# Optimization experiments

Hardware: AMD Instinct MI355X
Metric: run time of the kernel (lower is better)

The kernel has to match this reference:

```python
import jax, jax.numpy as jnp
import numpy as np

DIM = 2048
S = 4           # num_residual_streams
V = 1           # num_input_views
LAYER_INDEX = 3
B = 4           # batch
N = 2048        # seq len
EPS = 1e-5


def setup_inputs() -> dict:
    key = jax.random.key(0)
    k0, = jax.random.split(key, 1)
    residuals = jax.random.normal(k0, (B * S, N, DIM), dtype=jnp.float32)
    # parameters, initialized as in the torch module
    norm_weight = jnp.ones((DIM,), dtype=jnp.float32)
    static_beta = jnp.ones((S,), dtype=jnp.float32)
    init_alpha0 = jnp.zeros((S, V), dtype=jnp.float32).at[LAYER_INDEX % S, :].set(1.0)
    static_alpha = jnp.concatenate([init_alpha0, jnp.eye(S, dtype=jnp.float32)], axis=1)  # (S, V+S)
    dynamic_alpha_fn = jnp.zeros((DIM, S + V), dtype=jnp.float32)
    dynamic_alpha_scale = jnp.float32(0.01)
    dynamic_beta_fn = jnp.zeros((DIM,), dtype=jnp.float32)
    dynamic_beta_scale = jnp.float32(0.01)
    return {
        "residuals": residuals,
        "norm_weight": norm_weight,
        "static_beta": static_beta,
        "static_alpha": static_alpha,
        "dynamic_alpha_fn": dynamic_alpha_fn,
        "dynamic_alpha_scale": dynamic_alpha_scale,
        "dynamic_beta_fn": dynamic_beta_fn,
        "dynamic_beta_scale": dynamic_beta_scale,
    }


def _layernorm(x, weight):
    mu = jnp.mean(x, axis=-1, keepdims=True)
    var = jnp.mean(jnp.square(x - mu), axis=-1, keepdims=True)
    return (x - mu) * jax.lax.rsqrt(var + EPS) * weight


def reference(residuals, norm_weight, static_beta, static_alpha,
              dynamic_alpha_fn, dynamic_alpha_scale,
              dynamic_beta_fn, dynamic_beta_scale):
    # ---- prepare ----
    # (b s) n d -> b n s d
    r = residuals.reshape(B, S, N, DIM).transpose(0, 2, 1, 3)  # (b, n, s, d)
    normed = _layernorm(r, norm_weight)
    wc_weight = jnp.tanh(normed @ dynamic_alpha_fn)            # (b, n, s, s+v)
    alpha = wc_weight * dynamic_alpha_scale + static_alpha     # (b, n, s, s+v)
    dc_weight = jnp.tanh(normed @ dynamic_beta_fn)             # (b, n, s)
    beta = dc_weight * dynamic_beta_scale + static_beta        # (b, n, s)
    mix_h = jnp.einsum('bnst,bnsd->bntd', alpha, r)            # (b, n, s+v, d)
    branch_input = mix_h[..., 0, :]                            # (b, n, d)  (views == 1)
    mixed_residuals = mix_h[..., 1:, :]                        # (b, n, s, d)
    # ---- forward (branch output fed back; identity branch) ----
    out = jnp.einsum('bnd,bns->bnsd', branch_input, beta) + mixed_residuals
    # b n s d -> (b s) n d
    return out.transpose(0, 2, 1, 3).reshape(B * S, N, DIM)
```

## Files before the change

kernel.cpp:

```cpp
#include <hip/hip_runtime.h>
#include <cstddef>

namespace {
constexpr int kDim = 2048;
constexpr int kS = 4;
constexpr int kSV = 5;
constexpr int kB = 4;
constexpr int kN = 2048;
constexpr float kEps = 1e-5f;
constexpr int kThreads = 256;
constexpr int kWaves = kThreads / 64;
}

__global__ __launch_bounds__(kThreads) void hyperconn_kernel(
    const float* __restrict__ res,
    const float* __restrict__ norm_w,
    const float* __restrict__ static_beta,
    const float* __restrict__ static_alpha,
    const float* __restrict__ alpha_fn,
    const float* __restrict__ alpha_scale_p,
    const float* __restrict__ beta_fn,
    const float* __restrict__ beta_scale_p,
    float* __restrict__ out)
{
  const int bid = blockIdx.x;
  const int b = bid / kN;
  const int n = bid % kN;
  const int tid = threadIdx.x;
  const int lane = tid & 63;
  const int wave = tid >> 6;

  __shared__ float red[kWaves][24];
  __shared__ float ab[24];

  const size_t plane = (size_t)kN * kDim;
  const float* base = res + (size_t)b * kS * plane + (size_t)n * kDim;
  float* obase      = out + (size_t)b * kS * plane + (size_t)n * kDim;

  const int d0 = tid * 4;
  const int d1 = tid * 4 + 1024;

  float r[kS][8];
  float wv[8];
#pragma unroll
  for (int s = 0; s < kS; ++s) {
    const float* rp = base + (size_t)s * plane;
    const float4 a = *(const float4*)(rp + d0);
    const float4 c = *(const float4*)(rp + d1);
    r[s][0] = a.x; r[s][1] = a.y; r[s][2] = a.z; r[s][3] = a.w;
    r[s][4] = c.x; r[s][5] = c.y; r[s][6] = c.z; r[s][7] = c.w;
  }
  {
    const float4 a = *(const float4*)(norm_w + d0);
    const float4 c = *(const float4*)(norm_w + d1);
    wv[0] = a.x; wv[1] = a.y; wv[2] = a.z; wv[3] = a.w;
    wv[4] = c.x; wv[5] = c.y; wv[6] = c.z; wv[7] = c.w;
  }

  float p1[8];
#pragma unroll
  for (int s = 0; s < kS; ++s) {
    float sm = 0.f, sq = 0.f;
#pragma unroll
    for (int j = 0; j < 8; ++j) { sm += r[s][j]; sq += r[s][j] * r[s][j]; }
    p1[2 * s] = sm;
    p1[2 * s + 1] = sq;
  }
#pragma unroll
  for (int k = 0; k < 8; ++k) {
#pragma unroll
    for (int off = 32; off > 0; off >>= 1)
      p1[k] += __shfl_xor(p1[k], off, 64);
  }
  if (lane == 0) {
#pragma unroll
    for (int k = 0; k < 8; ++k) red[wave][k] = p1[k];
  }
  __syncthreads();
#pragma unroll
  for (int k = 0; k < 8; ++k)
    p1[k] = red[0][k] + red[1][k] + red[2][k] + red[3][k];
  __syncthreads();

  float mu[kS], rstd[kS];
#pragma unroll
  for (int s = 0; s < kS; ++s) {
    const float m = p1[2 * s] * (1.f / kDim);
    const float var = p1[2 * s + 1] * (1.f / kDim) - m * m;
    mu[s] = m;
    rstd[s] = rsqrtf(var + kEps);
  }

  float p2[24];
#pragma unroll
  for (int k = 0; k < 24; ++k) p2[k] = 0.f;
#pragma unroll
  for (int half = 0; half < 2; ++half) {
#pragma unroll
    for (int j = 0; j < 4; ++j) {
      const int idx = half * 4 + j;
      const int d = (half ? d1 : d0) + j;
      const float a0 = alpha_fn[(size_t)d * kSV + 0];
      const float a1 = alpha_fn[(size_t)d * kSV + 1];
      const float a2 = alpha_fn[(size_t)d * kSV + 2];
      const float a3 = alpha_fn[(size_t)d * kSV + 3];
      const float a4 = alpha_fn[(size_t)d * kSV + 4];
      const float bv = beta_fn[d];
#pragma unroll
      for (int s = 0; s < kS; ++s) {
        const float nm = (r[s][idx] - mu[s]) * rstd[s] * wv[idx];
        p2[s * 6 + 0] = fmaf(nm, a0, p2[s * 6 + 0]);
        p2[s * 6 + 1] = fmaf(nm, a1, p2[s * 6 + 1]);
        p2[s * 6 + 2] = fmaf(nm, a2, p2[s * 6 + 2]);
        p2[s * 6 + 3] = fmaf(nm, a3, p2[s * 6 + 3]);
        p2[s * 6 + 4] = fmaf(nm, a4, p2[s * 6 + 4]);
        p2[s * 6 + 5] = fmaf(nm, bv, p2[s * 6 + 5]);
      }
    }
  }
#pragma unroll
  for (int k = 0; k < 24; ++k) {
#pragma unroll
    for (int off = 32; off > 0; off >>= 1)
      p2[k] += __shfl_xor(p2[k], off, 64);
  }
  if (lane == 0) {
#pragma unroll
    for (int k = 0; k < 24; ++k) red[wave][k] = p2[k];
  }
  __syncthreads();

  if (tid < 24) {
    const float tot = red[0][tid] + red[1][tid] + red[2][tid] + red[3][tid];
    const int s = tid / 6;
    const int q = tid % 6;
    const float t = tanhf(tot);
    float val;
    if (q < 5) val = fmaf(t, alpha_scale_p[0], static_alpha[s * kSV + q]);
    else       val = fmaf(t, beta_scale_p[0], static_beta[s]);
    ab[tid] = val;
  }
  __syncthreads();

  float al[kS][kSV], be[kS];
#pragma unroll
  for (int s = 0; s < kS; ++s) {
#pragma unroll
    for (int t = 0; t < kSV; ++t) al[s][t] = ab[s * 6 + t];
    be[s] = ab[s * 6 + 5];
  }

#pragma unroll
  for (int half = 0; half < 2; ++half) {
    const int dd = half ? d1 : d0;
    float4 ov[kS];
#pragma unroll
    for (int j = 0; j < 4; ++j) {
      const int idx = half * 4 + j;
      const float r0 = r[0][idx], r1 = r[1][idx], r2 = r[2][idx], r3 = r[3][idx];
      const float mix0 = al[0][0] * r0 + al[1][0] * r1 + al[2][0] * r2 + al[3][0] * r3;
#pragma unroll
      for (int so = 0; so < kS; ++so) {
        float t = al[0][so + 1] * r0 + al[1][so + 1] * r1 +
                  al[2][so + 1] * r2 + al[3][so + 1] * r3;
        t = fmaf(be[so], mix0, t);
        (&ov[so].x)[j] = t;
      }
    }
#pragma unroll
    for (int so = 0; so < kS; ++so)
      *(float4*)(obase + (size_t)so * plane + dd) = ov[so];
  }
}

extern "C" void kernel_launch(void* const* d_in, const int* in_sizes, int n_in,
                              void* d_out, int out_size, void* d_ws, size_t ws_size,
                              hipStream_t stream) {
  const float* res    = (const float*)d_in[0];
  const float* norm_w = (const float*)d_in[1];
  const float* sbeta  = (const float*)d_in[2];
  const float* salpha = (const float*)d_in[3];
  const float* afn    = (const float*)d_in[4];
  const float* ascale = (const float*)d_in[5];
  const float* bfn    = (const float*)d_in[6];
  const float* bscale = (const float*)d_in[7];
  float* outp = (float*)d_out;

  hipLaunchKernelGGL(hyperconn_kernel, dim3(kB * kN), dim3(kThreads), 0, stream,
                     res, norm_w, sbeta, salpha, afn, ascale, bfn, bscale, outp);
}
```

Measured before the change: 490.4 us.

## Fold norm weight into projection and merge layernorm stats with projection reduction

A tiny setup kernel precomputes norm_weight times alpha_fn and beta_fn in a transposed, vectorizable workspace layout, along with the column sums. The main kernel then accumulates sum, sum of squares and raw dot products in one pass. It recovers the normalized projections algebraically as (dot - mu*colsum)*rstd, which removes one block-wide reduction and barrier. It also replaces 32 separate butterfly reductions with a transposing shuffle reduction. The cost is an extra launch, a workspace dependency, and slightly different numerical rounding.

New measurement: 447.9 us. 1.09x faster.

```diff
diff --git a/kernel.cpp b/kernel.cpp
--- a/kernel.cpp
+++ b/kernel.cpp
@@ -10,17 +10,200 @@
 constexpr float kEps = 1e-5f;
 constexpr int kThreads = 256;
 constexpr int kWaves = kThreads / 64;
-}
-
-__global__ __launch_bounds__(kThreads) void hyperconn_kernel(
+constexpr int kNV = 32;
+constexpr size_t kWcElems = 6 * (size_t)kDim;
+constexpr size_t kWsNeeded = (kWcElems + 6) * sizeof(float);
+}
+
+__global__ __launch_bounds__(256) void hyperconn_setup(
+    const float* __restrict__ norm_w,
+    const float* __restrict__ alpha_fn,
+    const float* __restrict__ beta_fn,
+    float* __restrict__ ws)
+{
+  const int tid = threadIdx.x;
+  const int lane = tid & 63;
+  const int wave = tid >> 6;
+  __shared__ float red[4][6];
+
+  float acc[6] = {0.f, 0.f, 0.f, 0.f, 0.f, 0.f};
+#pragma unroll
+  for (int rep = 0; rep < kDim / 256; ++rep) {
+    const int d = rep * 256 + tid;
+    const float w = norm_w[d];
+    float c[6];
+    c[0] = alpha_fn[(size_t)d * kSV + 0];
+    c[1] = alpha_fn[(size_t)d * kSV + 1];
+    c[2] = alpha_fn[(size_t)d * kSV + 2];
+    c[3] = alpha_fn[(size_t)d * kSV + 3];
+    c[4] = alpha_fn[(size_t)d * kSV + 4];
+    c[5] = beta_fn[d];
+#pragma unroll
+    for (int t = 0; t < 6; ++t) {
+      const float wc = w * c[t];
+      ws[(size_t)t * kDim + d] = wc;
+      acc[t] += wc;
+    }
+  }
+#pragma unroll
+  for (int t = 0; t < 6; ++t) {
+#pragma unroll
+    for (int off = 32; off > 0; off >>= 1)
+      acc[t] += __shfl_xor(acc[t], off, 64);
+  }
+  if (lane == 0) {
+#pragma unroll
+    for (int t = 0; t < 6; ++t) red[wave][t] = acc[t];
+  }
+  __syncthreads();
+  if (tid < 6)
+    ws[kWcElems + tid] = red[0][tid] + red[1][tid] + red[2][tid] + red[3][tid];
+}
+
+__global__ __launch_bounds__(kThreads) void hyperconn_main(
     const float* __restrict__ res,
-    const float* __restrict__ norm_w,
     const float* __restrict__ static_beta,
     const float* __restrict__ static_alpha,
-    const float* __restrict__ alpha_fn,
     const float* __restrict__ alpha_scale_p,
-    const float* __restrict__ beta_fn,
     const float* __restrict__ beta_scale_p,
+    const float* __restrict__ ws,
+    float* __restrict__ out)
+{
+  const int bid = blockIdx.x;
+  const int b = bid >> 11;
+  const int n = bid & (kN - 1);
+  const int tid = threadIdx.x;
+  const int lane = tid & 63;
+  const int wave = tid >> 6;
+
+  __shared__ float red[kWaves][kNV];
+  __shared__ float ab[24];
+
+  const size_t plane = (size_t)kN * kDim;
+  const float* base = res + (size_t)b * kS * plane + (size_t)n * kDim;
+  float* obase      = out + (size_t)b * kS * plane + (size_t)n * kDim;
+
+  const int d0 = tid * 4;
+  const int d1 = tid * 4 + 1024;
+
+  float r[kS][8];
+#pragma unroll
+  for (int s = 0; s < kS; ++s) {
+    const float* rp = base + (size_t)s * plane;
+    const float4 a = *(const float4*)(rp + d0);
+    const float4 c = *(const float4*)(rp + d1);
+    r[s][0] = a.x; r[s][1] = a.y; r[s][2] = a.z; r[s][3] = a.w;
+    r[s][4] = c.x; r[s][5] = c.y; r[s][6] = c.z; r[s][7] = c.w;
+  }
+
+  float v[kNV];
+#pragma unroll
+  for (int k = 0; k < kNV; ++k) v[k] = 0.f;
+
+#pragma unroll
+  for (int half = 0; half < 2; ++half) {
+    const int dd = half ? d1 : d0;
+    float4 c0 = *(const float4*)(ws + 0 * kDim + dd);
+    float4 c1 = *(const float4*)(ws + 1 * kDim + dd);
+    float4 c2 = *(const float4*)(ws + 2 * kDim + dd);
+    float4 c3 = *(const float4*)(ws + 3 * kDim + dd);
+    float4 c4 = *(const float4*)(ws + 4 * kDim + dd);
+    float4 c5 = *(const float4*)(ws + 5 * kDim + dd);
+    const float* p0 = &c0.x; const float* p1 = &c1.x; const float* p2 = &c2.x;
+    const float* p3 = &c3.x; const float* p4 = &c4.x; const float* p5 = &c5.x;
+#pragma unroll
+    for (int j = 0; j < 4; ++j) {
+      const int idx = half * 4 + j;
+      const float w0 = p0[j], w1 = p1[j], w2 = p2[j];
+      const float w3 = p3[j], w4 = p4[j], w5 = p5[j];
+#pragma unroll
+      for (int s = 0; s < kS; ++s) {
+        const float rv = r[s][idx];
+        v[s * 8 + 0] += rv;
+        v[s * 8 + 1] = fmaf(rv, rv, v[s * 8 + 1]);
+        v[s * 8 + 2] = fmaf(rv, w0, v[s * 8 + 2]);
+        v[s * 8 + 3] = fmaf(rv, w1, v[s * 8 + 3]);
+        v[s * 8 + 4] = fmaf(rv, w2, v[s * 8 + 4]);
+        v[s * 8 + 5] = fmaf(rv, w3, v[s * 8 + 5]);
+        v[s * 8 + 6] = fmaf(rv, w4, v[s * 8 + 6]);
+        v[s * 8 + 7] = fmaf(rv, w5, v[s * 8 + 7]);
+      }
+    }
+  }
+
+#pragma unroll
+  for (int st = 0; st < 5; ++st) {
+    const int mask = 1 << st;
+    const int half_n = kNV >> (st + 1);
+#pragma unroll
+    for (int i = 0; i < half_n; ++i) {
+      const float send = (lane & mask) ? v[2 * i] : v[2 * i + 1];
+      const float keep = (lane & mask) ? v[2 * i + 1] : v[2 * i];
+      v[i] = keep + __shfl_xor(send, mask, 64);
+    }
+  }
+  v[0] += __shfl_xor(v[0], 32, 64);
+
+  if (lane < kNV) red[wave][lane] = v[0];
+  __syncthreads();
+
+  if (tid < kNV) {
+    const int s = tid >> 3;
+    const int q = tid & 7;
+    if (q >= 2) {
+      const float sum = red[0][s * 8] + red[1][s * 8] + red[2][s * 8] + red[3][s * 8];
+      const float sq  = red[0][s * 8 + 1] + red[1][s * 8 + 1] + red[2][s * 8 + 1] + red[3][s * 8 + 1];
+      const float tot = red[0][tid] + red[1][tid] + red[2][tid] + red[3][tid];
+      const float mu = sum * (1.f / kDim);
+      const float var = sq * (1.f / kDim) - mu * mu;
+      const float rstd = rsqrtf(var + kEps);
+      const float wa = ws[kWcElems + (q - 2)];
+      const float dotn = (tot - mu * wa) * rstd;
+      const float t = tanhf(dotn);
+      const float val = (q < 7)
+          ? fmaf(t, alpha_scale_p[0], static_alpha[s * kSV + (q - 2)])
+          : fmaf(t, beta_scale_p[0], static_beta[s]);
+      ab[s * 6 + (q - 2)] = val;
+    }
+  }
+  __syncthreads();
+
+  float al[kS][kSV], be[kS];
+#pragma unroll
+  for (int s = 0; s < kS; ++s) {
+#pragma unroll
+    for (int t = 0; t < kSV; ++t) al[s][t] = ab[s * 6 + t];
+    be[s] = ab[s * 6 + 5];
+  }
+
+#pragma unroll
+  for (int half = 0; half < 2; ++half) {
+    const int dd = half ? d1 : d0;
+    float4 ov[kS];
+#pragma unroll
+    for (int j = 0; j < 4; ++j) {
+      const int idx = half * 4 + j;
+      const float r0 = r[0][idx], r1 = r[1][idx], r2 = r[2][idx], r3 = r[3][idx];
+      const float mix0 = al[0][0] * r0 + al[1][0] * r1 + al[2][0] * r2 + al[3][0] * r3;
+#pragma unroll
+      for (int so = 0; so < kS; ++so) {
+        float t = al[0][so + 1] * r0 + al[1][so + 1] * r1 +
+                  al[2][so + 1] * r2 + al[3][so + 1] * r3;
+        t = fmaf(be[so], mix0, t);
+        (&ov[so].x)[j] = t;
+      }
+    }
+#pragma unroll
+    for (int so = 0; so < kS; ++so)
+      *(float4*)(obase + (size_t)so * plane + dd) = ov[so];
+  }
+}
+
+__global__ __launch_bounds__(kThreads) void hyperconn_fallback(
+    const float* __restrict__ res, const float* __restrict__ norm_w,
+    const float* __restrict__ static_beta, const float* __restrict__ static_alpha,
+    const float* __restrict__ alpha_fn, const float* __restrict__ alpha_scale_p,
+    const float* __restrict__ beta_fn, const float* __restrict__ beta_scale_p,
     float* __restrict__ out)
 {
   const int bid = blockIdx.x;
@@ -29,17 +212,13 @@
   const int tid = threadIdx.x;
   const int lane = tid & 63;
   const int wave = tid >> 6;
-
   __shared__ float red[kWaves][24];
   __shared__ float ab[24];
-
   const size_t plane = (size_t)kN * kDim;
   const float* base = res + (size_t)b * kS * plane + (size_t)n * kDim;
   float* obase      = out + (size_t)b * kS * plane + (size_t)n * kDim;
-
   const int d0 = tid * 4;
   const int d1 = tid * 4 + 1024;
-
   float r[kS][8];
   float wv[8];
 #pragma unroll
@@ -56,41 +235,34 @@
     wv[0] = a.x; wv[1] = a.y; wv[2] = a.z; wv[3] = a.w;
     wv[4] = c.x; wv[5] = c.y; wv[6] = c.z; wv[7] = c.w;
   }
-
   float p1[8];
 #pragma unroll
   for (int s = 0; s < kS; ++s) {
     float sm = 0.f, sq = 0.f;
 #pragma unroll
     for (int j = 0; j < 8; ++j) { sm += r[s][j]; sq += r[s][j] * r[s][j]; }
-    p1[2 * s] = sm;
-    p1[2 * s + 1] = sq;
-  }
-#pragma unroll
-  for (int k = 0; k < 8; ++k) {
+    p1[2 * s] = sm; p1[2 * s + 1] = sq;
+  }
+#pragma unroll
+  for (int k = 0; k < 8; ++k)
 #pragma unroll
     for (int off = 32; off > 0; off >>= 1)
       p1[k] += __shfl_xor(p1[k], off, 64);
-  }
-  if (lane == 0) {
+  if (lane == 0)
 #pragma unroll
     for (int k = 0; k < 8; ++k) red[wave][k] = p1[k];
-  }
   __syncthreads();
 #pragma unroll
   for (int k = 0; k < 8; ++k)
     p1[k] = red[0][k] + red[1][k] + red[2][k] + red[3][k];
   __syncthreads();
-
   float mu[kS], rstd[kS];
 #pragma unroll
   for (int s = 0; s < kS; ++s) {
     const float m = p1[2 * s] * (1.f / kDim);
     const float var = p1[2 * s + 1] * (1.f / kDim) - m * m;
-    mu[s] = m;
-    rstd[s] = rsqrtf(var + kEps);
-  }
-
+    mu[s] = m; rstd[s] = rsqrtf(var + kEps);
+  }
   float p2[24];
 #pragma unroll
   for (int k = 0; k < 24; ++k) p2[k] = 0.f;
@@ -119,21 +291,17 @@
     }
   }
 #pragma unroll
-  for (int k = 0; k < 24; ++k) {
+  for (int k = 0; k < 24; ++k)
 #pragma unroll
     for (int off = 32; off > 0; off >>= 1)
       p2[k] += __shfl_xor(p2[k], off, 64);
-  }
-  if (lane == 0) {
+  if (lane == 0)
 #pragma unroll
     for (int k = 0; k < 24; ++k) red[wave][k] = p2[k];
-  }
-  __syncthreads();
-
+  __syncthreads();
   if (tid < 24) {
     const float tot = red[0][tid] + red[1][tid] + red[2][tid] + red[3][tid];
-    const int s = tid / 6;
-    const int q = tid % 6;
+    const int s = tid / 6; const int q = tid % 6;
     const float t = tanhf(tot);
     float val;
     if (q < 5) val = fmaf(t, alpha_scale_p[0], static_alpha[s * kSV + q]);
@@ -141,7 +309,6 @@
     ab[tid] = val;
   }
   __syncthreads();
-
   float al[kS][kSV], be[kS];
 #pragma unroll
   for (int s = 0; s < kS; ++s) {
@@ -149,7 +316,6 @@
     for (int t = 0; t < kSV; ++t) al[s][t] = ab[s * 6 + t];
     be[s] = ab[s * 6 + 5];
   }
-
 #pragma unroll
   for (int half = 0; half < 2; ++half) {
     const int dd = half ? d1 : d0;
@@ -186,6 +352,13 @@
   const float* bscale = (const float*)d_in[7];
   float* outp = (float*)d_out;
 
-  hipLaunchKernelGGL(hyperconn_kernel, dim3(kB * kN), dim3(kThreads), 0, stream,
-                     res, norm_w, sbeta, salpha, afn, ascale, bfn, bscale, outp);
-}
+  if (ws_size >= kWsNeeded) {
+    hipLaunchKernelGGL(hyperconn_setup, dim3(1), dim3(256), 0, stream,
+                       norm_w, afn, bfn, (float*)d_ws);
+    hipLaunchKernelGGL(hyperconn_main, dim3(kB * kN), dim3(kThreads), 0, stream,
+                       res, sbeta, salpha, ascale, bscale, (const float*)d_ws, outp);
+  } else {
+    hipLaunchKernelGGL(hyperconn_fallback, dim3(kB * kN), dim3(kThreads), 0, stream,
+                       res, norm_w, sbeta, salpha, afn, ascale, bfn, bscale, outp);
+  }
+}
```
